# Optimization experiments

Measured on AMD Instinct MI355X. Metric: run time of the kernel, lower is better.

Reference implementation:

```python
import jax, jax.numpy as jnp
import numpy as np

D_MODEL = 1024
N_HEADS = 16


def get_freqs(seq, n_dim):
    # standard RoPE angles: (seq, n_dim//2)
    inv = 1.0 / (10000.0 ** (jnp.arange(0, n_dim, 2, dtype=jnp.float32) / n_dim))
    pos = jnp.arange(seq, dtype=jnp.float32)
    return pos[:, None] * inv[None, :]


def rope(x, freq):
    # x: (batch, seq, heads, n_dim); interleaved-pair rotation
    xf = x.astype(jnp.float32)
    x1 = xf[..., 0::2]
    x2 = xf[..., 1::2]
    cos = jnp.cos(freq)[None, :, None, :]  # (1, seq, 1, n_dim//2)
    sin = jnp.sin(freq)[None, :, None, :]
    r1 = x1 * cos - x2 * sin
    r2 = x1 * sin + x2 * cos
    out = jnp.stack([r1, r2], axis=-1).reshape(x.shape)
    return out.astype(x.dtype)


def setup_inputs() -> dict:
    key = jax.random.key(0)
    k1, k2, k3, k4, k5 = jax.random.split(key, 5)
    batch, seq = 2, 2048
    x = jax.random.normal(k1, (batch, seq, D_MODEL), dtype=jnp.float16)
    scale = jnp.float16(0.02)
    qw = jax.random.normal(k2, (D_MODEL, D_MODEL), dtype=jnp.float16) * scale
    kw = jax.random.normal(k3, (D_MODEL, D_MODEL), dtype=jnp.float16) * scale
    vw = jax.random.normal(k4, (D_MODEL, D_MODEL), dtype=jnp.float16) * scale
    ow = jax.random.normal(k5, (D_MODEL, D_MODEL), dtype=jnp.float16) * scale
    return {"x": x, "qw": qw, "kw": kw, "vw": vw, "ow": ow}


def reference(x, qw, kw, vw, ow):
    batch, seq, dim = x.shape
    n_heads = N_HEADS
    n_dim = dim // n_heads

    Q = (x @ qw).reshape(batch, seq, n_heads, n_dim)
    K = (x @ kw).reshape(batch, seq, n_heads, n_dim)
    V = (x @ vw).reshape(batch, seq, n_heads, n_dim)

    freq = get_freqs(seq, n_dim)
    Q = rope(Q, freq)
    K = rope(K, freq)

    Q = jnp.transpose(Q, (0, 2, 1, 3))  # (b, h, s, d)
    K = jnp.transpose(K, (0, 2, 1, 3))
    V = jnp.transpose(V, (0, 2, 1, 3))

    score = (Q @ jnp.swapaxes(K, -1, -2)) / jnp.sqrt(jnp.float16(dim))
    score = score.astype(jnp.float32)
    mask = jnp.tril(jnp.ones((1, 1, seq, seq), dtype=jnp.float32))
    score = score - 1e10 * (1.0 - mask)
    weights = jax.nn.softmax(score, axis=-1)  # fp32 (b, h, s, s)
    attn = weights @ V.astype(jnp.float32)

    merged = jnp.transpose(attn, (0, 2, 1, 3)).reshape(batch, seq, dim)
    out = merged @ ow.astype(jnp.float32)
    return out
```

## Files before the change

kernel.cpp:

```cpp
#include <hip/hip_runtime.h>
#include <math.h>

typedef _Float16 f16x8 __attribute__((ext_vector_type(8)));
typedef _Float16 f16x4 __attribute__((ext_vector_type(4)));
typedef float f32x4 __attribute__((ext_vector_type(4)));

#define SEQ 2048
#define DM 1024
#define NH 16
#define HD 64
#define MTOT 4096

#define NEG_BIG (-30000.0f)

__device__ __forceinline__ void gl_lds16(const _Float16* g, _Float16* l) {
  __builtin_amdgcn_global_load_lds(
      (const __attribute__((address_space(1))) unsigned int*)g,
      (__attribute__((address_space(3))) unsigned int*)l, 16, 0, 0);
}

__global__ __launch_bounds__(256) void prep(const float* __restrict__ x,
                                            const float* __restrict__ qw,
                                            const float* __restrict__ kw,
                                            const float* __restrict__ vw,
                                            const float* __restrict__ ow,
                                            _Float16* __restrict__ x16,
                                            _Float16* __restrict__ wT) {
  const int z = blockIdx.z;
  const int t = threadIdx.x;
  if (z >= 4) {
    const int c = (z - 4) * 256 + blockIdx.y * 16 + blockIdx.x;
    const size_t base = (size_t)c * 8192;
#pragma unroll
    for (int rnd = 0; rnd < 4; ++rnd) {
      const size_t i = base + rnd * 2048 + t * 8;
      f32x4 a = *(const f32x4*)(x + i);
      f32x4 b = *(const f32x4*)(x + i + 4);
      f16x8 o;
#pragma unroll
      for (int j = 0; j < 4; ++j) { o[j] = (_Float16)a[j]; o[4 + j] = (_Float16)b[j]; }
      *(f16x8*)(x16 + i) = o;
    }
    return;
  }
  __shared__ float Ts[64][65];
  const float* srcs[4] = {qw, kw, vw, ow};
  const float* src = srcs[z];
  _Float16* dst = wT + (size_t)z * DM * DM;
  const int k0 = blockIdx.y * 64, n0 = blockIdx.x * 64;
  const int r = t >> 2, c4 = (t & 3) * 16;
  const float* sp = src + (size_t)(k0 + r) * DM + n0 + c4;
#pragma unroll
  for (int j = 0; j < 4; ++j) {
    f32x4 vv = *(const f32x4*)(sp + j * 4);
#pragma unroll
    for (int e = 0; e < 4; ++e) Ts[r][c4 + j * 4 + e] = vv[e];
  }
  __syncthreads();
  f16x8 o0, o1;
#pragma unroll
  for (int j = 0; j < 8; ++j) {
    o0[j] = (_Float16)Ts[c4 + j][r];
    o1[j] = (_Float16)Ts[c4 + 8 + j][r];
  }
  _Float16* dp = dst + (size_t)(n0 + r) * DM + k0 + c4;
  *(f16x8*)(dp) = o0;
  *(f16x8*)(dp + 8) = o1;
}

template <int BM, int BN, bool FUSED3, bool OUTF32, bool ROPE>
__global__ __launch_bounds__(256) void gemm_t(const _Float16* __restrict__ A,
                                              const _Float16* __restrict__ BT,
                                              void* __restrict__ Yv,
                                              int M, int K) {
  constexpr int WM = BM / 2, WN = BN / 2;
  constexpr int MI = WM / 16, NI = WN / 16;
  __shared__ _Float16 As[BM * 32];
  __shared__ _Float16 Bs[BN * 32];
  const int tid = threadIdx.x;
  const int lane = tid & 63;
  const int fl = lane & 15, fh = lane >> 4;
  const int wave = tid >> 6;
  const int m0 = blockIdx.y * BM;
  int n0 = blockIdx.x * BN;
  int mat = 0;
  const _Float16* Bp = BT;
  char* Yp = (char*)Yv;
  if (FUSED3) {
    mat = n0 >> 10;
    n0 &= 1023;
    Bp = BT + (size_t)mat * DM * DM;
    Yp += (size_t)mat * M * DM * (OUTF32 ? 4 : 2);
  }
  const int wm = (wave >> 1) * WM, wn = (wave & 1) * WN;

  const int l4 = lane >> 2, lc = (lane & 3) * 8;

  f32x4 acc[MI][NI] = {};

  for (int k0 = 0; k0 < K; k0 += 32) {
    __syncthreads();
#pragma unroll
    for (int j = wave; j < BM / 16; j += 4)
      gl_lds16(A + (size_t)(m0 + j * 16 + l4) * K + k0 + lc, &As[j * 16 * 32]);
#pragma unroll
    for (int j = wave; j < BN / 16; j += 4)
      gl_lds16(Bp + (size_t)(n0 + j * 16 + l4) * K + k0 + lc, &Bs[j * 16 * 32]);
    __syncthreads();
    f16x8 af[MI], bf[NI];
#pragma unroll
    for (int mi = 0; mi < MI; ++mi)
      af[mi] = *(const f16x8*)(&As[(wm + mi * 16 + fl) * 32 + fh * 8]);
#pragma unroll
    for (int ni = 0; ni < NI; ++ni)
      bf[ni] = *(const f16x8*)(&Bs[(wn + ni * 16 + fl) * 32 + fh * 8]);
#pragma unroll
    for (int mi = 0; mi < MI; ++mi)
#pragma unroll
      for (int ni = 0; ni < NI; ++ni)
        acc[mi][ni] = __builtin_amdgcn_mfma_f32_16x16x32_f16(af[mi], bf[ni], acc[mi][ni], 0, 0, 0);
  }

#pragma unroll
  for (int mi = 0; mi < MI; ++mi)
#pragma unroll
    for (int ni = 0; ni < NI; ++ni) {
      const int gm = m0 + wm + mi * 16 + fh * 4;
      const int gn = n0 + wn + ni * 16 + fl;
      if (ROPE && mat < 2) {
        const int d2 = (gn & 63) >> 1;
        const float inv = __powf(10000.0f, -(float)d2 * (1.0f / 32.0f));
        const float sgn = (gn & 1) ? 1.0f : -1.0f;
#pragma unroll
        for (int r = 0; r < 4; ++r) {
          const int s = (gm + r) & (SEQ - 1);
          float c, sn;
          __sincosf((float)s * inv, &sn, &c);
          const float v = acc[mi][ni][r];
          const float p = __shfl_xor(v, 1, 64);
          acc[mi][ni][r] = v * c + sgn * p * sn;
        }
      }
#pragma unroll
      for (int r = 0; r < 4; ++r) {
        if (OUTF32)
          ((float*)Yp)[(size_t)(gm + r) * DM + gn] = acc[mi][ni][r];
        else
          ((_Float16*)Yp)[(size_t)(gm + r) * DM + gn] = (_Float16)acc[mi][ni][r];
      }
    }
}

__device__ __forceinline__ void attn_tile(const _Float16 (*Ks)[72],
                                          const _Float16 (*Vt)[136],
                                          const f16x8 qf[2], f32x4 o_acc[4],
                                          float& m_r, float& l_r, int kv0,
                                          int qt, bool do_mask, int fl, int fh) {
  f32x4 s[8];
#pragma unroll
  for (int t = 0; t < 8; ++t) {
    f16x8 kf0 = *(const f16x8*)(&Ks[t * 16 + fl][fh * 8]);
    f16x8 kf1 = *(const f16x8*)(&Ks[t * 16 + fl][32 + fh * 8]);
    f32x4 z = {0.f, 0.f, 0.f, 0.f};
    z = __builtin_amdgcn_mfma_f32_16x16x32_f16(kf0, qf[0], z, 0, 0, 0);
    z = __builtin_amdgcn_mfma_f32_16x16x32_f16(kf1, qf[1], z, 0, 0, 0);
    s[t] = z;
  }
  const int qg = qt + fl;
  if (do_mask) {
#pragma unroll
    for (int t = 0; t < 8; ++t)
#pragma unroll
      for (int r = 0; r < 4; ++r)
        if (kv0 + t * 16 + fh * 4 + r > qg) s[t][r] = NEG_BIG;
  }
  float mx = s[0][0];
#pragma unroll
  for (int t = 0; t < 8; ++t)
#pragma unroll
    for (int r = 0; r < 4; ++r) mx = fmaxf(mx, s[t][r]);
  mx = fmaxf(mx, __shfl_xor(mx, 16, 64));
  mx = fmaxf(mx, __shfl_xor(mx, 32, 64));
  float mn = m_r;
  if (__any(mx > m_r + 8.0f)) {
    mn = fmaxf(m_r, mx);
    const float a = __expf(m_r - mn);
    l_r *= a;
#pragma unroll
    for (int mt = 0; mt < 4; ++mt)
#pragma unroll
      for (int r = 0; r < 4; ++r) o_acc[mt][r] *= a;
    m_r = mn;
  }
  float rs = 0.f;
  f16x4 pb[8];
#pragma unroll
  for (int t = 0; t < 8; ++t) {
    float p0 = __expf(s[t][0] - mn);
    float p1 = __expf(s[t][1] - mn);
    float p2 = __expf(s[t][2] - mn);
    float p3 = __expf(s[t][3] - mn);
    rs += (p0 + p1) + (p2 + p3);
    f16x4 pk = {(_Float16)p0, (_Float16)p1, (_Float16)p2, (_Float16)p3};
    pb[t] = pk;
  }
  rs += __shfl_xor(rs, 16, 64);
  rs += __shfl_xor(rs, 32, 64);
  l_r += rs;
#pragma unroll
  for (int mt = 0; mt < 4; ++mt)
#pragma unroll
    for (int t = 0; t < 8; ++t) {
      f16x4 va = *(const f16x4*)(&Vt[mt * 16 + fl][t * 16 + fh * 4]);
      o_acc[mt] = __builtin_amdgcn_mfma_f32_16x16x16f16(va, pb[t], o_acc[mt], 0, 0, 0);
    }
}

__global__ __launch_bounds__(512) void attn_kernel(const _Float16* __restrict__ Q,
                                                   const _Float16* __restrict__ K,
                                                   const _Float16* __restrict__ V,
                                                   _Float16* __restrict__ O) {
  __shared__ _Float16 Ks[128][72];
  __shared__ _Float16 Vt[64][136];

  const int tid = threadIdx.x;
  const int lane = tid & 63;
  const int fl = lane & 15, fh = lane >> 4;
  const int wave = tid >> 6;
  const int lin = blockIdx.y * 8 + blockIdx.x;
  const int w = (lin & 7) * 32 + (lin >> 3);
  const int p = w & 7;
  const int bh = w >> 3;
  const int b = bh >> 4, h = bh & 15;
  const int qt_lo = p * 128 + wave * 16;
  const int qt_hi = (15 - p) * 128 + wave * 16;

  const _Float16* Qb = Q + (size_t)b * SEQ * DM + h * HD;
  const _Float16* Kb = K + (size_t)b * SEQ * DM + h * HD;
  const _Float16* Vb = V + (size_t)b * SEQ * DM + h * HD;

  const _Float16 hs = (_Float16)0.03125f;
  f16x8 qlo[2], qhi[2];
#pragma unroll
  for (int kh = 0; kh < 2; ++kh) {
    qlo[kh] = *(const f16x8*)(Qb + (size_t)(qt_lo + fl) * DM + kh * 32 + fh * 8);
    qhi[kh] = *(const f16x8*)(Qb + (size_t)(qt_hi + fl) * DM + kh * 32 + fh * 8);
#pragma unroll
    for (int j = 0; j < 8; ++j) { qlo[kh][j] *= hs; qhi[kh][j] *= hs; }
  }

  f32x4 o_lo[4] = {}, o_hi[4] = {};
  float m_lo = NEG_BIG, l_lo = 0.f, m_hi = NEG_BIG, l_hi = 0.f;

  const int sr = tid >> 3, e = tid & 7, sc8 = e * 8;
  const int cmax = 15 - p;

  f16x8 k0v = *(const f16x8*)(Kb + (size_t)(sr) * DM + sc8);
  f16x8 k1v = *(const f16x8*)(Kb + (size_t)(64 + sr) * DM + sc8);
  f16x8 v0v = *(const f16x8*)(Vb + (size_t)(sr) * DM + sc8);
  f16x8 v1v = *(const f16x8*)(Vb + (size_t)(64 + sr) * DM + sc8);

  for (int c = 0; c <= cmax; ++c) {
    const int kv0 = c * 128;
    __syncthreads();
    *(f16x8*)(&Ks[sr][sc8]) = k0v;
    *(f16x8*)(&Ks[64 + sr][sc8]) = k1v;
#pragma unroll
    for (int t = 0; t < 8; ++t) {
      const int jj = (t + e) & 7;
      Vt[sc8 + jj][sr] = v0v[jj];
      Vt[sc8 + jj][64 + sr] = v1v[jj];
    }
    __syncthreads();

    if (c < cmax) {
      const int kn = kv0 + 128;
      k0v = *(const f16x8*)(Kb + (size_t)(kn + sr) * DM + sc8);
      k1v = *(const f16x8*)(Kb + (size_t)(kn + 64 + sr) * DM + sc8);
      v0v = *(const f16x8*)(Vb + (size_t)(kn + sr) * DM + sc8);
      v1v = *(const f16x8*)(Vb + (size_t)(kn + 64 + sr) * DM + sc8);
    }

    attn_tile(Ks, Vt, qhi, o_hi, m_hi, l_hi, kv0, qt_hi, c == cmax, fl, fh);
    if (c <= p)
      attn_tile(Ks, Vt, qlo, o_lo, m_lo, l_lo, kv0, qt_lo, c == p, fl, fh);
  }

  {
    const float il = 1.0f / l_lo;
    _Float16* Op = O + ((size_t)b * SEQ + qt_lo + fl) * DM + h * HD;
#pragma unroll
    for (int mt = 0; mt < 4; ++mt) {
      f16x4 ov = {(_Float16)(o_lo[mt][0] * il), (_Float16)(o_lo[mt][1] * il),
                  (_Float16)(o_lo[mt][2] * il), (_Float16)(o_lo[mt][3] * il)};
      *(f16x4*)(Op + mt * 16 + fh * 4) = ov;
    }
  }
  {
    const float il = 1.0f / l_hi;
    _Float16* Op = O + ((size_t)b * SEQ + qt_hi + fl) * DM + h * HD;
#pragma unroll
    for (int mt = 0; mt < 4; ++mt) {
      f16x4 ov = {(_Float16)(o_hi[mt][0] * il), (_Float16)(o_hi[mt][1] * il),
                  (_Float16)(o_hi[mt][2] * il), (_Float16)(o_hi[mt][3] * il)};
      *(f16x4*)(Op + mt * 16 + fh * 4) = ov;
    }
  }
}

extern "C" void kernel_launch(void* const* d_in, const int* in_sizes, int n_in,
                              void* d_out, int out_size, void* d_ws, size_t ws_size,
                              hipStream_t stream) {
  const float* x = (const float*)d_in[0];
  const float* qw = (const float*)d_in[1];
  const float* kw = (const float*)d_in[2];
  const float* vw = (const float*)d_in[3];
  const float* ow = (const float*)d_in[4];
  float* out = (float*)d_out;

  const size_t MD = (size_t)MTOT * DM;
  _Float16* x16 = (_Float16*)d_ws;
  _Float16* wT = x16 + MD;
  _Float16* Qw = wT + 4 * (size_t)DM * DM;
  _Float16* Kw = Qw + MD;
  _Float16* Vw = Kw + MD;
  _Float16* Mw = x16;

  prep<<<dim3(16, 16, 6), 256, 0, stream>>>(x, qw, kw, vw, ow, x16, wT);

  gemm_t<128, 128, true, false, true><<<dim3(24, MTOT / 128), 256, 0, stream>>>(
      x16, wT, Qw, MTOT, DM);

  attn_kernel<<<dim3(8, 32), 512, 0, stream>>>(Qw, Kw, Vw, Mw);

  gemm_t<64, 128, false, true, false><<<dim3(8, MTOT / 64), 256, 0, stream>>>(
      Mw, wT + 3 * (size_t)DM * DM, out, MTOT, DM);
}
```

Before: 196.4 us.

## Use exp2 softmax with log2e folded into Q scale and interleave both QK tiles

Folds log2(e) into the Q prescale so the softmax can use the native exp2 instruction instead of __expf, and raises the lazy-rescale threshold to match the base-2 domain. Splits attn_tile into a QK stage and a softmax+PV stage so that, when both query tiles are active, both QK MFMA batches are issued before either softmax, giving more independent work to overlap. It also changes the LDS transpose swizzle for V to cut bank conflicts. In exchange it holds two score arrays live at once, which raises register pressure, and folding the constant into the fp16 scale slightly changes rounding.

```diff
diff --git a/kernel.cpp b/kernel.cpp
--- a/kernel.cpp
+++ b/kernel.cpp
@@ -12,6 +12,10 @@
 #define MTOT 4096
 
 #define NEG_BIG (-30000.0f)
+
+__device__ __forceinline__ float ex2(float x) {
+  return __builtin_amdgcn_exp2f(x);
+}
 
 __device__ __forceinline__ void gl_lds16(const _Float16* g, _Float16* l) {
   __builtin_amdgcn_global_load_lds(
@@ -151,12 +155,9 @@
     }
 }
 
-__device__ __forceinline__ void attn_tile(const _Float16 (*Ks)[72],
-                                          const _Float16 (*Vt)[136],
-                                          const f16x8 qf[2], f32x4 o_acc[4],
-                                          float& m_r, float& l_r, int kv0,
-                                          int qt, bool do_mask, int fl, int fh) {
-  f32x4 s[8];
+__device__ __forceinline__ void qk_tile(const _Float16 (*Ks)[72],
+                                        const f16x8 qf[2], f32x4 s[8],
+                                        int fl, int fh) {
 #pragma unroll
   for (int t = 0; t < 8; ++t) {
     f16x8 kf0 = *(const f16x8*)(&Ks[t * 16 + fl][fh * 8]);
@@ -166,7 +167,12 @@
     z = __builtin_amdgcn_mfma_f32_16x16x32_f16(kf1, qf[1], z, 0, 0, 0);
     s[t] = z;
   }
-  const int qg = qt + fl;
+}
+
+__device__ __forceinline__ void sm_pv(const _Float16 (*Vt)[136], f32x4 s[8],
+                                      f32x4 o_acc[4], float& m_r, float& l_r,
+                                      int kv0, int qg, bool do_mask, int fl,
+                                      int fh) {
   if (do_mask) {
 #pragma unroll
     for (int t = 0; t < 8; ++t)
@@ -182,9 +188,9 @@
   mx = fmaxf(mx, __shfl_xor(mx, 16, 64));
   mx = fmaxf(mx, __shfl_xor(mx, 32, 64));
   float mn = m_r;
-  if (__any(mx > m_r + 8.0f)) {
+  if (__any(mx > m_r + 11.5f)) {
     mn = fmaxf(m_r, mx);
-    const float a = __expf(m_r - mn);
+    const float a = ex2(m_r - mn);
     l_r *= a;
 #pragma unroll
     for (int mt = 0; mt < 4; ++mt)
@@ -196,10 +202,10 @@
   f16x4 pb[8];
 #pragma unroll
   for (int t = 0; t < 8; ++t) {
-    float p0 = __expf(s[t][0] - mn);
-    float p1 = __expf(s[t][1] - mn);
-    float p2 = __expf(s[t][2] - mn);
-    float p3 = __expf(s[t][3] - mn);
+    float p0 = ex2(s[t][0] - mn);
+    float p1 = ex2(s[t][1] - mn);
+    float p2 = ex2(s[t][2] - mn);
+    float p3 = ex2(s[t][3] - mn);
     rs += (p0 + p1) + (p2 + p3);
     f16x4 pk = {(_Float16)p0, (_Float16)p1, (_Float16)p2, (_Float16)p3};
     pb[t] = pk;
@@ -239,7 +245,7 @@
   const _Float16* Kb = K + (size_t)b * SEQ * DM + h * HD;
   const _Float16* Vb = V + (size_t)b * SEQ * DM + h * HD;
 
-  const _Float16 hs = (_Float16)0.03125f;
+  const _Float16 hs = (_Float16)(0.03125f * 1.44269504f);
   f16x8 qlo[2], qhi[2];
 #pragma unroll
   for (int kh = 0; kh < 2; ++kh) {
@@ -253,6 +259,7 @@
   float m_lo = NEG_BIG, l_lo = 0.f, m_hi = NEG_BIG, l_hi = 0.f;
 
   const int sr = tid >> 3, e = tid & 7, sc8 = e * 8;
+  const int jbase = (e + ((sr & 1) << 2)) & 7;
   const int cmax = 15 - p;
 
   f16x8 k0v = *(const f16x8*)(Kb + (size_t)(sr) * DM + sc8);
@@ -267,7 +274,7 @@
     *(f16x8*)(&Ks[64 + sr][sc8]) = k1v;
 #pragma unroll
     for (int t = 0; t < 8; ++t) {
-      const int jj = (t + e) & 7;
+      const int jj = (t + jbase) & 7;
       Vt[sc8 + jj][sr] = v0v[jj];
       Vt[sc8 + jj][64 + sr] = v1v[jj];
     }
@@ -281,9 +288,17 @@
       v1v = *(const f16x8*)(Vb + (size_t)(kn + 64 + sr) * DM + sc8);
     }
 
-    attn_tile(Ks, Vt, qhi, o_hi, m_hi, l_hi, kv0, qt_hi, c == cmax, fl, fh);
-    if (c <= p)
-      attn_tile(Ks, Vt, qlo, o_lo, m_lo, l_lo, kv0, qt_lo, c == p, fl, fh);
+    if (c <= p) {
+      f32x4 s_hi[8], s_lo[8];
+      qk_tile(Ks, qhi, s_hi, fl, fh);
+      qk_tile(Ks, qlo, s_lo, fl, fh);
+      sm_pv(Vt, s_hi, o_hi, m_hi, l_hi, kv0, 0, false, fl, fh);
+      sm_pv(Vt, s_lo, o_lo, m_lo, l_lo, kv0, qt_lo + fl, c == p, fl, fh);
+    } else {
+      f32x4 s_hi[8];
+      qk_tile(Ks, qhi, s_hi, fl, fh);
+      sm_pv(Vt, s_hi, o_hi, m_hi, l_hi, kv0, qt_hi + fl, c == cmax, fl, fh);
+    }
   }
 
   {
```

After: 201.3 us. 1.02x slower.
